# Kernel tuning notes

Measured on AMD Instinct MI355X. Metric: run time of the kernel, lower is better.

## Reference

```python
import jax, jax.numpy as jnp
import numpy as np

B, S, E, H, D = 4, 2048, 1024, 8, 256  # batch, seq, embed_dim, heads, hidden_units


def setup_inputs() -> dict:
    key = jax.random.key(0)
    ks = jax.random.split(key, 9)
    scale = 0.02
    return {
        "inputA": jax.random.normal(ks[0], (B, S, E), dtype=jnp.float32),
        "WQ": jax.random.normal(ks[1], (H, E, D), dtype=jnp.float32) * scale,
        "bQ": jnp.zeros((H, D), dtype=jnp.float32),
        "WK": jax.random.normal(ks[2], (H, E, D), dtype=jnp.float32) * scale,
        "bK": jnp.zeros((H, D), dtype=jnp.float32),
        "WV": jax.random.normal(ks[3], (H, E, D), dtype=jnp.float32) * scale,
        "bV": jnp.zeros((H, D), dtype=jnp.float32),
        "WZ": jax.random.normal(ks[4], (H * D, E), dtype=jnp.float32) * scale,
        "bZ": jnp.zeros((E,), dtype=jnp.float32),
    }


def reference(inputA, WQ, bQ, WK, bK, WV, bV, WZ, bZ):
    # Per-head Linear -> ReLU (dropout=0 -> identity); heads stacked on axis h.
    Q = jax.nn.relu(jnp.einsum('bse,hed->bhsd', inputA, WQ) + bQ[None, :, None, :])
    K = jax.nn.relu(jnp.einsum('bse,hed->bhsd', inputA, WK) + bK[None, :, None, :])
    V = jax.nn.relu(jnp.einsum('bse,hed->bhsd', inputA, WV) + bV[None, :, None, :])
    # scores[b,h,s,t] ; torch bmm output was [B, S, T] per head
    scores = jnp.einsum('bhsd,bhtd->bhst', Q, K) / jnp.sqrt(jnp.float32(E))
    # double softmax: torch dim=1 (query axis s) then dim=2 (key axis t)
    A = jax.nn.softmax(scores, axis=2)
    A = jax.nn.softmax(A, axis=3)
    Z = jnp.einsum('bhst,bhtd->bhsd', A, V)
    # concat heads along feature dim (head order matches torch cat)
    Zall = Z.transpose(0, 2, 1, 3).reshape(B, S, H * D)
    return Zall @ WZ + bZ
```

## Files before the change

### kernel.cpp

```cpp
#include <hip/hip_runtime.h>

typedef __attribute__((ext_vector_type(8))) short short8;
typedef __attribute__((ext_vector_type(4))) float f32x4;

constexpr int B_ = 4, S_ = 2048, E_ = 1024, H_ = 8, D_ = 256;
constexpr int HD_ = H_ * D_;
constexpr int BS_ = B_ * S_;
constexpr int BH_ = B_ * H_;
constexpr float INV_SQRT_E = 0.03125f;

__device__ __forceinline__ unsigned short f2bf(float f) {
    union { float f; unsigned u; } x; x.f = f;
    unsigned r = (x.u + 0x7fffu + ((x.u >> 16) & 1u)) >> 16;
    return (unsigned short)r;
}

__device__ __forceinline__ unsigned pk2(float a, float b) {
    return (unsigned)f2bf(a) | ((unsigned)f2bf(b) << 16);
}

__device__ __forceinline__ void gl_lds16(const void* g, void* lds) {
    __builtin_amdgcn_global_load_lds((const __attribute__((address_space(1))) void*)g,
                                     (__attribute__((address_space(3))) void*)lds, 16, 0, 0);
}

__global__ __launch_bounds__(256) void cast_k(const float* __restrict__ src,
                                              unsigned short* __restrict__ dst, int n4) {
    int i = blockIdx.x * 256 + threadIdx.x;
    if (i >= n4) return;
    float4 v = reinterpret_cast<const float4*>(src)[i];
    ushort4 o;
    o.x = f2bf(v.x); o.y = f2bf(v.y); o.z = f2bf(v.z); o.w = f2bf(v.w);
    reinterpret_cast<ushort4*>(dst)[i] = o;
}

__global__ __launch_bounds__(256) void tcast_k(const float* __restrict__ src,
                                               unsigned short* __restrict__ dst, int R, int C) {
    __shared__ float tile[32][33];
    int b = blockIdx.z;
    const float* s = src + (size_t)b * R * C;
    unsigned short* d = dst + (size_t)b * R * C;
    int c0 = blockIdx.x * 32, r0 = blockIdx.y * 32;
    int tx = threadIdx.x, ty = threadIdx.y;
#pragma unroll
    for (int i = 0; i < 4; ++i)
        tile[ty + i * 8][tx] = s[(size_t)(r0 + ty + i * 8) * C + c0 + tx];
    __syncthreads();
#pragma unroll
    for (int i = 0; i < 4; ++i)
        d[(size_t)(c0 + ty + i * 8) * R + r0 + tx] = f2bf(tile[tx][ty + i * 8]);
}

__global__ __launch_bounds__(256) void tbf_k(const unsigned short* __restrict__ src,
                                             unsigned short* __restrict__ dst) {
    __shared__ unsigned short tile[32][33];
    int bh = blockIdx.z;
    int d0 = blockIdx.x * 32, s0 = blockIdx.y * 32;
    int tx = threadIdx.x, ty = threadIdx.y;
#pragma unroll
    for (int i = 0; i < 4; ++i)
        tile[ty + i * 8][tx] = src[((size_t)bh * S_ + s0 + ty + i * 8) * D_ + d0 + tx];
    __syncthreads();
#pragma unroll
    for (int i = 0; i < 4; ++i)
        dst[((size_t)bh * D_ + d0 + ty + i * 8) * S_ + s0 + tx] = tile[tx][ty + i * 8];
}

__global__ __launch_bounds__(256) void gemm_qkv_k(const unsigned short* __restrict__ A,
                                                  const unsigned short* __restrict__ Bt,
                                                  const float* __restrict__ bias,
                                                  unsigned short* __restrict__ out) {
    __shared__ __align__(16) unsigned short As[128 * 32];
    __shared__ __align__(16) unsigned short Bs[128 * 32];
    const int tid = threadIdx.x;
    const int wave = tid >> 6, lane = tid & 63;
    const int quad = lane >> 4, l15 = lane & 15;
    const int wm = wave >> 1, wn = wave & 1;
    const int m0 = blockIdx.y * 128, n0 = blockIdx.x * 128;
    const int c1 = tid, c2 = tid + 256;
    const int r1 = c1 >> 2, kc1 = (c1 & 3) * 8;
    const int r2 = c2 >> 2, kc2 = (c2 & 3) * 8;
    char* aB1 = (char*)As + wave * 1024; char* aB2 = aB1 + 4096;
    char* bB1 = (char*)Bs + wave * 1024; char* bB2 = bB1 + 4096;
    const unsigned short* a1 = A + (size_t)(m0 + r1) * E_ + kc1;
    const unsigned short* a2 = A + (size_t)(m0 + r2) * E_ + kc2;
    const unsigned short* b1 = Bt + (size_t)(n0 + r1) * E_ + kc1;
    const unsigned short* b2 = Bt + (size_t)(n0 + r2) * E_ + kc2;
    f32x4 acc[4][4] = {};
    for (int k0 = 0; k0 < E_; k0 += 32) {
        __syncthreads();
        gl_lds16(a1 + k0, aB1);
        gl_lds16(a2 + k0, aB2);
        gl_lds16(b1 + k0, bB1);
        gl_lds16(b2 + k0, bB2);
        __syncthreads();
        short8 af[4], bf[4];
        const short* Ass = (const short*)As;
        const short* Bss = (const short*)Bs;
#pragma unroll
        for (int f = 0; f < 4; ++f) {
            af[f] = *(const short8*)&Ass[(wm * 64 + f * 16 + l15) * 32 + quad * 8];
            bf[f] = *(const short8*)&Bss[(wn * 64 + f * 16 + l15) * 32 + quad * 8];
        }
#pragma unroll
        for (int fm = 0; fm < 4; ++fm)
#pragma unroll
            for (int fn = 0; fn < 4; ++fn)
                acc[fm][fn] = __builtin_amdgcn_mfma_f32_16x16x32_bf16(af[fm], bf[fn], acc[fm][fn], 0, 0, 0);
    }
#pragma unroll
    for (int fm = 0; fm < 4; ++fm) {
        int mbase = m0 + wm * 64 + fm * 16 + quad * 4;
#pragma unroll
        for (int fn = 0; fn < 4; ++fn) {
            int n = n0 + wn * 64 + fn * 16 + l15;
            int h = n >> 8, d = n & 255;
            float bv = bias[n];
#pragma unroll
            for (int r = 0; r < 4; ++r) {
                int m = mbase + r;
                int b = m >> 11, s = m & 2047;
                float v = fmaxf(acc[fm][fn][r] + bv, 0.0f);
                out[((size_t)(b * H_ + h) * S_ + s) * D_ + d] = f2bf(v);
            }
        }
    }
}

__global__ __launch_bounds__(256) void gemm_out_k(const unsigned short* __restrict__ A,
                                                  const unsigned short* __restrict__ Bt,
                                                  const float* __restrict__ bias,
                                                  float* __restrict__ out) {
    __shared__ __align__(16) unsigned short As[128 * 32];
    __shared__ __align__(16) unsigned short Bs[128 * 32];
    const int tid = threadIdx.x;
    const int wave = tid >> 6, lane = tid & 63;
    const int quad = lane >> 4, l15 = lane & 15;
    const int wm = wave >> 1, wn = wave & 1;
    const int m0 = blockIdx.y * 128, n0 = blockIdx.x * 128;
    const int c1 = tid, c2 = tid + 256;
    const int r1 = c1 >> 2, kc1 = (c1 & 3) * 8;
    const int r2 = c2 >> 2, kc2 = (c2 & 3) * 8;
    char* aB1 = (char*)As + wave * 1024; char* aB2 = aB1 + 4096;
    char* bB1 = (char*)Bs + wave * 1024; char* bB2 = bB1 + 4096;
    const unsigned short* a1 = A + (size_t)(m0 + r1) * HD_ + kc1;
    const unsigned short* a2 = A + (size_t)(m0 + r2) * HD_ + kc2;
    const unsigned short* b1 = Bt + (size_t)(n0 + r1) * HD_ + kc1;
    const unsigned short* b2 = Bt + (size_t)(n0 + r2) * HD_ + kc2;
    f32x4 acc[4][4] = {};
    for (int k0 = 0; k0 < HD_; k0 += 32) {
        __syncthreads();
        gl_lds16(a1 + k0, aB1);
        gl_lds16(a2 + k0, aB2);
        gl_lds16(b1 + k0, bB1);
        gl_lds16(b2 + k0, bB2);
        __syncthreads();
        short8 af[4], bf[4];
        const short* Ass = (const short*)As;
        const short* Bss = (const short*)Bs;
#pragma unroll
        for (int f = 0; f < 4; ++f) {
            af[f] = *(const short8*)&Ass[(wm * 64 + f * 16 + l15) * 32 + quad * 8];
            bf[f] = *(const short8*)&Bss[(wn * 64 + f * 16 + l15) * 32 + quad * 8];
        }
#pragma unroll
        for (int fm = 0; fm < 4; ++fm)
#pragma unroll
            for (int fn = 0; fn < 4; ++fn)
                acc[fm][fn] = __builtin_amdgcn_mfma_f32_16x16x32_bf16(af[fm], bf[fn], acc[fm][fn], 0, 0, 0);
    }
#pragma unroll
    for (int fm = 0; fm < 4; ++fm) {
        int mbase = m0 + wm * 64 + fm * 16 + quad * 4;
#pragma unroll
        for (int fn = 0; fn < 4; ++fn) {
            int n = n0 + wn * 64 + fn * 16 + l15;
            float bv = bias[n];
#pragma unroll
            for (int r = 0; r < 4; ++r)
                out[(size_t)(mbase + r) * E_ + n] = acc[fm][fn][r] + bv;
        }
    }
}

__global__ __launch_bounds__(512, 2) void colsum_k(const unsigned short* __restrict__ Q,
                                                   const unsigned short* __restrict__ K,
                                                   float* __restrict__ invLcol) {
    __shared__ float part[8][64];
    const int tid = threadIdx.x;
    const int wave = tid >> 6, lane = tid & 63;
    const int quad = lane >> 4, l15 = lane & 15;
    const int tg = wave >> 2, sg = wave & 3;
    const int p = blockIdx.x;
    const int bh = (p & 7) + 8 * ((p >> 3) >> 4);
    const int t0 = ((p >> 3) & 15) * 128;
    const unsigned short* Qh = Q + (size_t)bh * S_ * D_;
    const unsigned short* Kh = K + (size_t)bh * S_ * D_;
    short8 kf[32];
#pragma unroll
    for (int kc = 0; kc < 8; ++kc)
#pragma unroll
        for (int fm = 0; fm < 4; ++fm)
            kf[kc * 4 + fm] = *(const short8*)&Kh[(size_t)(t0 + tg * 64 + fm * 16 + l15) * D_ + kc * 32 + quad * 8];
    float rl[4][4] = {};
    const unsigned short* Qw = Qh + (size_t)(sg * 16 + l15) * D_ + quad * 8;
    short8 qf[8];
#pragma unroll
    for (int kc = 0; kc < 8; ++kc) qf[kc] = *(const short8*)&Qw[kc * 32];
    for (int s0 = 0; s0 < S_; s0 += 64) {
        f32x4 acc[4] = {};
#pragma unroll
        for (int kc = 0; kc < 8; ++kc)
#pragma unroll
            for (int fm = 0; fm < 4; ++fm)
                acc[fm] = __builtin_amdgcn_mfma_f32_16x16x32_bf16(kf[kc * 4 + fm], qf[kc], acc[fm], 0, 0, 0);
        int sn = (s0 + 64) & (S_ - 1);
#pragma unroll
        for (int kc = 0; kc < 8; ++kc)
            qf[kc] = *(const short8*)&Qw[(size_t)sn * D_ + kc * 32];
#pragma unroll
        for (int fm = 0; fm < 4; ++fm)
#pragma unroll
            for (int r = 0; r < 4; ++r)
                rl[fm][r] += __expf(acc[fm][r] * INV_SQRT_E);
    }
#pragma unroll
    for (int fm = 0; fm < 4; ++fm)
#pragma unroll
        for (int r = 0; r < 4; ++r) {
            float v = rl[fm][r];
            v += __shfl_xor(v, 1); v += __shfl_xor(v, 2);
            v += __shfl_xor(v, 4); v += __shfl_xor(v, 8);
            if (l15 == 0) part[wave][fm * 16 + quad * 4 + r] = v;
        }
    __syncthreads();
    if (tid < 128) {
        int tg2 = tid >> 6, i = tid & 63;
        float s = part[tg2 * 4 + 0][i] + part[tg2 * 4 + 1][i] +
                  part[tg2 * 4 + 2][i] + part[tg2 * 4 + 3][i];
        invLcol[(size_t)bh * S_ + t0 + tid] = 1.0f / s;
    }
}

__global__ __launch_bounds__(256, 2) void flash12_k(const unsigned short* __restrict__ Q,
                                                    const unsigned short* __restrict__ K,
                                                    const unsigned short* __restrict__ Vt,
                                                    const float* __restrict__ invLcol,
                                                    unsigned short* __restrict__ Zall) {
    __shared__ __align__(16) char KsB[2 * 16 * 1024];
    __shared__ __align__(16) char VsB[2 * 16 * 1024];
    const int tid = threadIdx.x;
    const int wave = tid >> 6, lane = tid & 63;
    const int q = lane >> 4, l15 = lane & 15;
    const int p = blockIdx.x;
    const int bh = (p & 7) + 8 * ((p >> 3) >> 4);
    const int s0 = ((p >> 3) & 15) * 128;
    const int bb = bh >> 3, hh = bh & 7;
    const unsigned short* Qh = Q + (size_t)bh * S_ * D_;
    const unsigned short* Kh = K + (size_t)bh * S_ * D_;
    const unsigned short* Vh = Vt + (size_t)bh * D_ * S_;
    const float* Lc = invLcol + (size_t)bh * S_;
    const int sbase = s0 + wave * 32;
    const int krow = 8 * (l15 >> 2) + (l15 & 3);

    const unsigned short* Qw0 = Qh + (size_t)(sbase + l15) * D_ + q * 8;
    const unsigned short* Qw1 = Qw0 + (size_t)16 * D_;

    f32x4 zacc[2][16] = {};
    float rsacc[2] = {0.f, 0.f};

#pragma unroll
    for (int i = 0; i < 4; ++i) {
        const int seg = wave * 4 + i;
        const int kc = seg >> 1, sub = seg & 1;
        gl_lds16(Kh + (size_t)(sub * 4 + krow) * D_ + kc * 32 + q * 8, KsB + seg * 1024);
        gl_lds16(Vh + (size_t)(seg * 16 + l15) * S_ + q * 8, VsB + seg * 1024);
    }
    __syncthreads();

    for (int c = 0; c < 64; ++c) {
        const int t0 = c * 32;
        const char* Kcur = KsB + (c & 1) * 16384;
        const char* Vcur = VsB + (c & 1) * 16384;
        if (c < 63) {
            const int tn = t0 + 32;
            char* Knxt = KsB + ((c & 1) ^ 1) * 16384;
            char* Vnxt = VsB + ((c & 1) ^ 1) * 16384;
#pragma unroll
            for (int i = 0; i < 4; ++i) {
                const int seg = wave * 4 + i;
                const int kc = seg >> 1, sub = seg & 1;
                gl_lds16(Kh + (size_t)(tn + sub * 4 + krow) * D_ + kc * 32 + q * 8, Knxt + seg * 1024);
                gl_lds16(Vh + (size_t)(seg * 16 + l15) * S_ + tn + q * 8, Vnxt + seg * 1024);
            }
        }
        f32x4 acc[2][2] = {};
#pragma unroll
        for (int kc = 0; kc < 8; ++kc) {
            short8 kf0 = *(const short8*)(Kcur + (kc * 2 + 0) * 1024 + lane * 16);
            short8 kf1 = *(const short8*)(Kcur + (kc * 2 + 1) * 1024 + lane * 16);
            short8 qf0 = *(const short8*)&Qw0[kc * 32];
            short8 qf1 = *(const short8*)&Qw1[kc * 32];
            acc[0][0] = __builtin_amdgcn_mfma_f32_16x16x32_bf16(kf0, qf0, acc[0][0], 0, 0, 0);
            acc[0][1] = __builtin_amdgcn_mfma_f32_16x16x32_bf16(kf1, qf0, acc[0][1], 0, 0, 0);
            acc[1][0] = __builtin_amdgcn_mfma_f32_16x16x32_bf16(kf0, qf1, acc[1][0], 0, 0, 0);
            acc[1][1] = __builtin_amdgcn_mfma_f32_16x16x32_bf16(kf1, qf1, acc[1][1], 0, 0, 0);
        }
        const float4 iv0 = *(const float4*)(Lc + t0 + 8 * q);
        const float4 iv1 = *(const float4*)(Lc + t0 + 8 * q + 4);
        short8 pa[2];
#pragma unroll
        for (int st = 0; st < 2; ++st) {
            const f32x4 a0 = acc[st][0], a1 = acc[st][1];
            float e0 = __expf(__expf(a0[0] * INV_SQRT_E) * iv0.x);
            float e1 = __expf(__expf(a0[1] * INV_SQRT_E) * iv0.y);
            float e2 = __expf(__expf(a0[2] * INV_SQRT_E) * iv0.z);
            float e3 = __expf(__expf(a0[3] * INV_SQRT_E) * iv0.w);
            float e4 = __expf(__expf(a1[0] * INV_SQRT_E) * iv1.x);
            float e5 = __expf(__expf(a1[1] * INV_SQRT_E) * iv1.y);
            float e6 = __expf(__expf(a1[2] * INV_SQRT_E) * iv1.z);
            float e7 = __expf(__expf(a1[3] * INV_SQRT_E) * iv1.w);
            rsacc[st] += ((e0 + e1) + (e2 + e3)) + ((e4 + e5) + (e6 + e7));
            union { short8 v; unsigned u[4]; } P;
            P.u[0] = pk2(e0, e1);
            P.u[1] = pk2(e2, e3);
            P.u[2] = pk2(e4, e5);
            P.u[3] = pk2(e6, e7);
            pa[st] = P.v;
        }
#pragma unroll
        for (int dt = 0; dt < 16; ++dt) {
            short8 vb = *(const short8*)(Vcur + dt * 1024 + lane * 16);
            zacc[0][dt] = __builtin_amdgcn_mfma_f32_16x16x32_bf16(pa[0], vb, zacc[0][dt], 0, 0, 0);
            zacc[1][dt] = __builtin_amdgcn_mfma_f32_16x16x32_bf16(pa[1], vb, zacc[1][dt], 0, 0, 0);
        }
        __syncthreads();
    }
#pragma unroll
    for (int st = 0; st < 2; ++st) {
        float rs = rsacc[st];
        rs += __shfl_xor(rs, 16);
        rs += __shfl_xor(rs, 32);
#pragma unroll
        for (int r = 0; r < 4; ++r) {
            const float inv = 1.0f / __shfl(rs, q * 4 + r);
            const size_t rowoff = (size_t)(bb * S_ + sbase + st * 16 + q * 4 + r) * HD_ + hh * D_;
#pragma unroll
            for (int dt = 0; dt < 16; ++dt)
                Zall[rowoff + dt * 16 + l15] = f2bf(zacc[st][dt][r] * inv);
        }
    }
}

extern "C" void kernel_launch(void* const* d_in, const int* in_sizes, int n_in,
                              void* d_out, int out_size, void* d_ws, size_t ws_size,
                              hipStream_t stream) {
    const float* Ain = (const float*)d_in[0];
    const float* WQ = (const float*)d_in[1];
    const float* bQ = (const float*)d_in[2];
    const float* WK = (const float*)d_in[3];
    const float* bK = (const float*)d_in[4];
    const float* WV = (const float*)d_in[5];
    const float* bV = (const float*)d_in[6];
    const float* WZ = (const float*)d_in[7];
    const float* bZ = (const float*)d_in[8];
    float* out = (float*)d_out;

    char* ws = (char*)d_ws;
    size_t off = 0;
    auto alloc = [&](size_t bytes) {
        char* p = ws + off;
        off += (bytes + 255) & ~(size_t)255;
        return p;
    };
    unsigned short* Abf = (unsigned short*)alloc((size_t)BS_ * E_ * 2);
    unsigned short* Wqt = (unsigned short*)alloc((size_t)H_ * D_ * E_ * 2);
    unsigned short* Wkt = (unsigned short*)alloc((size_t)H_ * D_ * E_ * 2);
    unsigned short* Wvt = (unsigned short*)alloc((size_t)H_ * D_ * E_ * 2);
    unsigned short* Wzt = (unsigned short*)alloc((size_t)E_ * HD_ * 2);
    unsigned short* Qb = (unsigned short*)alloc((size_t)BH_ * S_ * D_ * 2);
    unsigned short* Kb = (unsigned short*)alloc((size_t)BH_ * S_ * D_ * 2);
    unsigned short* Vb = (unsigned short*)alloc((size_t)BH_ * S_ * D_ * 2);
    unsigned short* Vtb = (unsigned short*)alloc((size_t)BH_ * S_ * D_ * 2);
    unsigned short* Zb = (unsigned short*)alloc((size_t)BS_ * HD_ * 2);
    float* Lc = (float*)alloc((size_t)BH_ * S_ * 4);

    dim3 tb(32, 8);
    cast_k<<<(BS_ * E_ / 4 + 255) / 256, 256, 0, stream>>>(Ain, Abf, BS_ * E_ / 4);
    tcast_k<<<dim3(D_ / 32, E_ / 32, H_), tb, 0, stream>>>(WQ, Wqt, E_, D_);
    tcast_k<<<dim3(D_ / 32, E_ / 32, H_), tb, 0, stream>>>(WK, Wkt, E_, D_);
    tcast_k<<<dim3(D_ / 32, E_ / 32, H_), tb, 0, stream>>>(WV, Wvt, E_, D_);
    tcast_k<<<dim3(E_ / 32, HD_ / 32, 1), tb, 0, stream>>>(WZ, Wzt, HD_, E_);

    gemm_qkv_k<<<dim3(HD_ / 128, BS_ / 128), 256, 0, stream>>>(Abf, Wqt, bQ, Qb);
    gemm_qkv_k<<<dim3(HD_ / 128, BS_ / 128), 256, 0, stream>>>(Abf, Wkt, bK, Kb);
    gemm_qkv_k<<<dim3(HD_ / 128, BS_ / 128), 256, 0, stream>>>(Abf, Wvt, bV, Vb);

    tbf_k<<<dim3(D_ / 32, S_ / 32, BH_), tb, 0, stream>>>(Vb, Vtb);

    colsum_k<<<dim3(BH_ * S_ / 128), 512, 0, stream>>>(Qb, Kb, Lc);
    flash12_k<<<dim3(BH_ * S_ / 128), 256, 0, stream>>>(Qb, Kb, Vtb, Lc, Zb);

    gemm_out_k<<<dim3(E_ / 128, BS_ / 128), 256, 0, stream>>>(Zb, Wzt, bZ, out);
}
```

Baseline: 667.9 us.

## Rewrite QKV GEMM with 256x256 tiles, double-buffered LDS and XOR swizzle

Replaces the 128x128 tile, 4-wave QKV projection GEMM with a 256x256 tile, 8-wave kernel that processes K in steps of 64. Shared-memory tiles are double-buffered, so the next K slice is fetched by global-to-LDS loads while MFMAs run on the current one, and the prologue sync plus one barrier per iteration replace the two per iteration. An XOR swizzle on the LDS layout is meant to avoid bank conflicts on the fragment reads. The larger tile raises arithmetic intensity but uses 128KB of LDS and many more accumulator registers per block, which limits occupancy, and the grid drops to 256 blocks per GEMM.

```diff
diff --git a/kernel.cpp b/kernel.cpp
--- a/kernel.cpp
+++ b/kernel.cpp
@@ -66,51 +66,72 @@
         dst[((size_t)bh * D_ + d0 + ty + i * 8) * S_ + s0 + tx] = tile[tx][ty + i * 8];
 }
 
-__global__ __launch_bounds__(256) void gemm_qkv_k(const unsigned short* __restrict__ A,
-                                                  const unsigned short* __restrict__ Bt,
-                                                  const float* __restrict__ bias,
-                                                  unsigned short* __restrict__ out) {
-    __shared__ __align__(16) unsigned short As[128 * 32];
-    __shared__ __align__(16) unsigned short Bs[128 * 32];
+__global__ __launch_bounds__(512, 2) void gemm_qkv256_k(const unsigned short* __restrict__ A,
+                                                        const unsigned short* __restrict__ Bt,
+                                                        const float* __restrict__ bias,
+                                                        unsigned short* __restrict__ out) {
+    __shared__ __align__(16) unsigned short As[2][256 * 64];
+    __shared__ __align__(16) unsigned short Bs[2][256 * 64];
     const int tid = threadIdx.x;
     const int wave = tid >> 6, lane = tid & 63;
     const int quad = lane >> 4, l15 = lane & 15;
-    const int wm = wave >> 1, wn = wave & 1;
-    const int m0 = blockIdx.y * 128, n0 = blockIdx.x * 128;
-    const int c1 = tid, c2 = tid + 256;
-    const int r1 = c1 >> 2, kc1 = (c1 & 3) * 8;
-    const int r2 = c2 >> 2, kc2 = (c2 & 3) * 8;
-    char* aB1 = (char*)As + wave * 1024; char* aB2 = aB1 + 4096;
-    char* bB1 = (char*)Bs + wave * 1024; char* bB2 = bB1 + 4096;
-    const unsigned short* a1 = A + (size_t)(m0 + r1) * E_ + kc1;
-    const unsigned short* a2 = A + (size_t)(m0 + r2) * E_ + kc2;
-    const unsigned short* b1 = Bt + (size_t)(n0 + r1) * E_ + kc1;
-    const unsigned short* b2 = Bt + (size_t)(n0 + r2) * E_ + kc2;
-    f32x4 acc[4][4] = {};
-    for (int k0 = 0; k0 < E_; k0 += 32) {
+    const int wm = wave >> 2, wn = wave & 3;
+    const int lrow = lane >> 3, lc = lane & 7;
+    const int p = blockIdx.x;
+    const int n0 = (p & 7) * 256;
+    const int m0 = (p >> 3) * 256;
+    int aoff[4], boff[4];
+#pragma unroll
+    for (int i = 0; i < 4; ++i) {
+        int rA = m0 + (wave * 4 + i) * 8 + lrow;
+        int rB = n0 + (wave * 4 + i) * 8 + lrow;
+        aoff[i] = rA * E_ + (lc ^ lrow) * 8;
+        boff[i] = rB * E_ + (lc ^ lrow) * 8;
+    }
+    f32x4 acc[8][4] = {};
+#pragma unroll
+    for (int i = 0; i < 4; ++i) {
+        gl_lds16(A + aoff[i], (char*)As + (wave * 4 + i) * 1024);
+        gl_lds16(Bt + boff[i], (char*)Bs + (wave * 4 + i) * 1024);
+    }
+    __syncthreads();
+    const int v0 = (quad ^ (l15 & 7)) * 16;
+    const int arow = (wm * 128 + l15) * 128;
+    const int brow = (wn * 64 + l15) * 128;
+    for (int k0 = 0; k0 < E_; k0 += 64) {
+        const int cur = (k0 >> 6) & 1;
+        if (k0 + 64 < E_) {
+            char* An = (char*)As + (cur ^ 1) * 32768;
+            char* Bn = (char*)Bs + (cur ^ 1) * 32768;
+#pragma unroll
+            for (int i = 0; i < 4; ++i) {
+                gl_lds16(A + aoff[i] + k0 + 64, An + (wave * 4 + i) * 1024);
+                gl_lds16(Bt + boff[i] + k0 + 64, Bn + (wave * 4 + i) * 1024);
+            }
+        }
+        const char* Ac = (const char*)As + cur * 32768;
+        const char* Bc = (const char*)Bs + cur * 32768;
+#pragma unroll
+        for (int kcc = 0; kcc < 2; ++kcc) {
+            const int vk = v0 ^ (kcc << 6);
+            short8 af[8], bf[4];
+#pragma unroll
+            for (int fm = 0; fm < 8; ++fm)
+                af[fm] = *(const short8*)(Ac + arow + fm * 2048 + vk);
+#pragma unroll
+            for (int fn = 0; fn < 4; ++fn)
+                bf[fn] = *(const short8*)(Bc + brow + fn * 2048 + vk);
+#pragma unroll
+            for (int fm = 0; fm < 8; ++fm)
+#pragma unroll
+                for (int fn = 0; fn < 4; ++fn)
+                    acc[fm][fn] = __builtin_amdgcn_mfma_f32_16x16x32_bf16(af[fm], bf[fn], acc[fm][fn], 0, 0, 0);
+        }
         __syncthreads();
-        gl_lds16(a1 + k0, aB1);
-        gl_lds16(a2 + k0, aB2);
-        gl_lds16(b1 + k0, bB1);
-        gl_lds16(b2 + k0, bB2);
-        __syncthreads();
-        short8 af[4], bf[4];
-        const short* Ass = (const short*)As;
-        const short* Bss = (const short*)Bs;
-#pragma unroll
-        for (int f = 0; f < 4; ++f) {
-            af[f] = *(const short8*)&Ass[(wm * 64 + f * 16 + l15) * 32 + quad * 8];
-            bf[f] = *(const short8*)&Bss[(wn * 64 + f * 16 + l15) * 32 + quad * 8];
-        }
-#pragma unroll
-        for (int fm = 0; fm < 4; ++fm)
-#pragma unroll
-            for (int fn = 0; fn < 4; ++fn)
-                acc[fm][fn] = __builtin_amdgcn_mfma_f32_16x16x32_bf16(af[fm], bf[fn], acc[fm][fn], 0, 0, 0);
-    }
-#pragma unroll
-    for (int fm = 0; fm < 4; ++fm) {
-        int mbase = m0 + wm * 64 + fm * 16 + quad * 4;
+    }
+#pragma unroll
+    for (int fm = 0; fm < 8; ++fm) {
+        int mbase = m0 + wm * 128 + fm * 16 + quad * 4;
 #pragma unroll
         for (int fn = 0; fn < 4; ++fn) {
             int n = n0 + wn * 64 + fn * 16 + l15;
@@ -392,9 +413,9 @@
     tcast_k<<<dim3(D_ / 32, E_ / 32, H_), tb, 0, stream>>>(WV, Wvt, E_, D_);
     tcast_k<<<dim3(E_ / 32, HD_ / 32, 1), tb, 0, stream>>>(WZ, Wzt, HD_, E_);
 
-    gemm_qkv_k<<<dim3(HD_ / 128, BS_ / 128), 256, 0, stream>>>(Abf, Wqt, bQ, Qb);
-    gemm_qkv_k<<<dim3(HD_ / 128, BS_ / 128), 256, 0, stream>>>(Abf, Wkt, bK, Kb);
-    gemm_qkv_k<<<dim3(HD_ / 128, BS_ / 128), 256, 0, stream>>>(Abf, Wvt, bV, Vb);
+    gemm_qkv256_k<<<dim3((BS_ / 256) * (HD_ / 256)), 512, 0, stream>>>(Abf, Wqt, bQ, Qb);
+    gemm_qkv256_k<<<dim3((BS_ / 256) * (HD_ / 256)), 512, 0, stream>>>(Abf, Wkt, bK, Kb);
+    gemm_qkv256_k<<<dim3((BS_ / 256) * (HD_ / 256)), 512, 0, stream>>>(Abf, Wvt, bV, Vb);
 
     tbf_k<<<dim3(D_ / 32, S_ / 32, BH_), tb, 0, stream>>>(Vb, Vtb);
 
```

After: 638.4 us. 4.4% less time.
